# Kernel tuning notes

Hardware: AMD Instinct MI355X
Metric: run time of the kernel (lower is better)

## Reference

```python
import jax, jax.numpy as jnp
import numpy as np

N = 100000
E = 1600000
F_IN = 602
NHID = 128
N_CLS = 41


def setup_inputs() -> dict:
    key = jax.random.key(0)
    k1, k2, k3, k4 = jax.random.split(key, 4)
    x = jax.random.normal(k1, (N, F_IN), dtype=jnp.float32)
    edge_index = jax.random.randint(k2, (2, E), 0, N, dtype=jnp.int64)
    # Glorot-style scaled weights
    W1 = jax.random.normal(k3, (F_IN, NHID), dtype=jnp.float32) * (1.0 / np.sqrt(F_IN))
    b1 = jnp.zeros((NHID,), dtype=jnp.float32)
    W2 = jax.random.normal(k4, (NHID, N_CLS), dtype=jnp.float32) * (1.0 / np.sqrt(NHID))
    b2 = jnp.zeros((N_CLS,), dtype=jnp.float32)
    return {"x": x, "edge_index": edge_index, "W1": W1, "b1": b1, "W2": W2, "b2": b2}


def reference(x, edge_index, W1, b1, W2, b2):
    n = x.shape[0]
    loop = jnp.arange(n, dtype=edge_index.dtype)
    # PyG GCNConv: add self-loops, symmetric normalization D^-1/2 (A+I) D^-1/2
    src = jnp.concatenate([edge_index[0], loop])  # [E+N]
    dst = jnp.concatenate([edge_index[1], loop])  # [E+N]
    ones = jnp.ones(src.shape[0], dtype=x.dtype)
    deg = jax.ops.segment_sum(ones, dst, num_segments=n)  # in-degree incl self-loop
    dinv = jnp.where(deg > 0, jax.lax.rsqrt(deg), 0.0)
    norm = dinv[src] * dinv[dst]  # [E+N]

    def conv(h, W, b):
        h = h @ W  # transform first (smaller feature dim for gather)
        msg = h[src] * norm[:, None]  # gather + scale
        return jax.ops.segment_sum(msg, dst, num_segments=n) + b  # scatter-add

    h = jax.nn.relu(conv(x, W1, b1))
    # dropout is identity in eval mode
    out = conv(h, W2, b2)
    return jax.nn.log_softmax(out, axis=1)
```

## Files before the change

### kernel.cpp

```cpp
#include <hip/hip_runtime.h>
#include <math.h>

#define GK 602
#define GH 128
#define GC 41
#define GCP 48
#define KPAD 608
#define NKT 19

typedef __bf16 bf16x8 __attribute__((ext_vector_type(8)));
typedef float f32x16 __attribute__((ext_vector_type(16)));

__device__ __forceinline__ unsigned short f2bf(float f) {
    __bf16 b = (__bf16)f;
    return __builtin_bit_cast(unsigned short, b);
}
__device__ __forceinline__ float bf2f(unsigned short u) {
    return __uint_as_float((unsigned int)u << 16);
}
__device__ __forceinline__ float bflo(unsigned int u) { return __uint_as_float(u << 16); }
__device__ __forceinline__ float bfhi(unsigned int u) { return __uint_as_float(u & 0xffff0000u); }


__global__ void k_hist(const int* __restrict__ dst, int* __restrict__ counts, int E) {
    int e = blockIdx.x * 256 + threadIdx.x;
    if (e < E) atomicAdd(&counts[dst[e]], 1);
}

__global__ void k_scan_a(const int* __restrict__ counts, int* __restrict__ row_ptr,
                         int* __restrict__ bsum, int n) {
    __shared__ int wsum[4];
    int t = threadIdx.x;
    int lane = t & 63;
    int wv = t >> 6;
    int base = blockIdx.x * 1024 + t * 4;
    int v[4];
    int s = 0;
#pragma unroll
    for (int j = 0; j < 4; ++j) {
        int idx = base + j;
        v[j] = (idx < n) ? counts[idx] : 0;
        s += v[j];
    }
    int incl = s;
#pragma unroll
    for (int o = 1; o < 64; o <<= 1) {
        int x = __shfl_up(incl, o);
        if (lane >= o) incl += x;
    }
    if (lane == 63) wsum[wv] = incl;
    __syncthreads();
    int woff = 0;
#pragma unroll
    for (int i = 0; i < 3; ++i) woff += (i < wv) ? wsum[i] : 0;
    if (t == 255) bsum[blockIdx.x] = woff + incl;
    int off = woff + incl - s;
#pragma unroll
    for (int j = 0; j < 4; ++j) {
        int idx = base + j;
        if (idx < n) row_ptr[idx] = off;
        off += v[j];
    }
}

__global__ void k_scan_b(int* __restrict__ bsum, int nb) {
    __shared__ int sh[256];
    int t = threadIdx.x;
    int v = (t < nb) ? bsum[t] : 0;
    sh[t] = v;
    __syncthreads();
    for (int o = 1; o < 256; o <<= 1) {
        int x = (t >= o) ? sh[t - o] : 0;
        __syncthreads();
        sh[t] += x;
        __syncthreads();
    }
    if (t < nb) bsum[t] = sh[t] - v;
}

__global__ void k_scan_c(int* __restrict__ row_ptr, const int* __restrict__ bsum,
                         const int* __restrict__ counts, float* __restrict__ dinv,
                         int* __restrict__ cursor, int n, int E) {
    int i = blockIdx.x * 256 + threadIdx.x;
    if (i < n) {
        int rp = row_ptr[i] + bsum[i >> 10];
        row_ptr[i] = rp;
        cursor[i] = rp;
        dinv[i] = rsqrtf((float)(counts[i] + 1));
    }
    if (i == 0) row_ptr[n] = E;
}

__global__ void k_fill(const int* __restrict__ src, const int* __restrict__ dst,
                       const float* __restrict__ dinv,
                       int* __restrict__ cursor, int2* __restrict__ meta, int E) {
    int e = blockIdx.x * 256 + threadIdx.x;
    if (e < E) {
        int s = src[e];
        int d = dst[e];
        int p = atomicAdd(&cursor[d], 1);
        float w = dinv[s] * dinv[d];
        meta[p] = make_int2(s, __float_as_int(w));
    }
}


__global__ void k_prepW1F(const float* __restrict__ W1, unsigned short* __restrict__ W1F) {
    int i = blockIdx.x * 256 + threadIdx.x;
    if (i >= NKT * 4096) return;
    int kt = i >> 12;
    int r  = i & 4095;
    int nt = r >> 10;
    int r2 = r & 1023;
    int bs = r2 >> 9;
    int r3 = r2 & 511;
    int ln = r3 >> 3;
    int j  = r3 & 7;
    int col = 32 * nt + (ln & 31);
    int k   = 32 * kt + 16 * bs + 8 * (ln >> 5) + j;
    float v = (k < GK) ? W1[(size_t)k * GH + col] : 0.f;
    W1F[i] = f2bf(v);
}


struct AF { float4 v0, v1, v2, v3; };

__device__ __forceinline__ AF loadA(const float* __restrict__ xr, int kb, bool tail) {
    AF r;
    if (!tail) {
        r.v0 = *(const float4*)(xr + kb);
        r.v1 = *(const float4*)(xr + kb + 4);
        r.v2 = *(const float4*)(xr + kb + 16);
        r.v3 = *(const float4*)(xr + kb + 20);
    } else {
        float tv[8], tw[8];
#pragma unroll
        for (int j = 0; j < 8; ++j) {
            int k0_ = kb + j;
            int k1_ = kb + 16 + j;
            tv[j] = (k0_ < GK) ? xr[k0_] : 0.f;
            tw[j] = (k1_ < GK) ? xr[k1_] : 0.f;
        }
        r.v0 = make_float4(tv[0], tv[1], tv[2], tv[3]);
        r.v1 = make_float4(tv[4], tv[5], tv[6], tv[7]);
        r.v2 = make_float4(tw[0], tw[1], tw[2], tw[3]);
        r.v3 = make_float4(tw[4], tw[5], tw[6], tw[7]);
    }
    return r;
}

__device__ __forceinline__ bf16x8 cvt8(float4 a, float4 b) {
    bf16x8 r;
    r[0] = (__bf16)a.x; r[1] = (__bf16)a.y; r[2] = (__bf16)a.z; r[3] = (__bf16)a.w;
    r[4] = (__bf16)b.x; r[5] = (__bf16)b.y; r[6] = (__bf16)b.z; r[7] = (__bf16)b.w;
    return r;
}

__global__ __launch_bounds__(256, 4) void k_gemm1_mfma(const float* __restrict__ X,
                                                       const unsigned short* __restrict__ W1F,
                                                       unsigned short* __restrict__ Y, int M) {
    int tid = threadIdx.x;
    int lane = tid & 63;
    int w = tid >> 6;
    int rowBase = blockIdx.x * 64 + (w & 1) * 32;
    int cg = w >> 1;
    int grow_base = rowBase + (lane & 31);
    int arow = (grow_base < M) ? grow_base : (M - 1);
    const float* xr = X + (size_t)arow * GK;
    int kh = (lane >> 5) * 8;

    f32x16 acc[2];
#pragma unroll
    for (int c = 0; c < 2; ++c)
#pragma unroll
        for (int i = 0; i < 16; ++i) acc[c][i] = 0.f;

    const unsigned short* Wb = W1F + (size_t)lane * 8 + (size_t)cg * 2048;

    AF a0 = loadA(xr, kh, false);
    AF a1 = loadA(xr, kh + 32, false);

    for (int t = 0; t < NKT; ++t) {
        AF a2;
        if (t + 2 < NKT) a2 = loadA(xr, kh + 32 * (t + 2), (t + 2) == (NKT - 1));
        else             a2 = a1;

        const unsigned short* Wt = Wb + (size_t)t * 4096;
        bf16x8 af0 = cvt8(a0.v0, a0.v1);
        bf16x8 af1 = cvt8(a0.v2, a0.v3);

        bf16x8 b00 = *(const bf16x8*)(Wt);
        bf16x8 b10 = *(const bf16x8*)(Wt + 1024);
        acc[0] = __builtin_amdgcn_mfma_f32_32x32x16_bf16(af0, b00, acc[0], 0, 0, 0);
        acc[1] = __builtin_amdgcn_mfma_f32_32x32x16_bf16(af0, b10, acc[1], 0, 0, 0);

        bf16x8 b01 = *(const bf16x8*)(Wt + 512);
        bf16x8 b11 = *(const bf16x8*)(Wt + 1024 + 512);
        acc[0] = __builtin_amdgcn_mfma_f32_32x32x16_bf16(af1, b01, acc[0], 0, 0, 0);
        acc[1] = __builtin_amdgcn_mfma_f32_32x32x16_bf16(af1, b11, acc[1], 0, 0, 0);

        a0 = a1;
        a1 = a2;
    }

#pragma unroll
    for (int c = 0; c < 2; ++c) {
        int nt = 2 * cg + c;
#pragma unroll
        for (int reg = 0; reg < 16; ++reg) {
            int rrow = (reg & 3) + 8 * (reg >> 2) + 4 * (lane >> 5);
            int grow = rowBase + rrow;
            int gcol = 32 * nt + (lane & 31);
            if (grow < M) Y[(size_t)grow * GH + gcol] = f2bf(acc[c][reg]);
        }
    }
}


__global__ __launch_bounds__(256) void k_agg1(const unsigned int* __restrict__ H,
                                              unsigned int* __restrict__ O,
                                              const int* __restrict__ row_ptr,
                                              const int2* __restrict__ meta,
                                              const float* __restrict__ dinv,
                                              const float* __restrict__ bias, int n) {
    int wv = threadIdx.x >> 6;
    int lane = threadIdx.x & 63;
    int d = blockIdx.x * 4 + wv;
    if (d >= n) return;
    float dd = dinv[d];
    int beg = row_ptr[d], end = row_ptr[d + 1];
    unsigned int v = H[(size_t)d * 64 + lane];
    float sw = dd * dd;
    float a0 = sw * bflo(v);
    float a1 = sw * bfhi(v);
    int e = beg;
    for (; e + 16 <= end; e += 16) {
        int2 m[16];
        unsigned int u[16];
#pragma unroll
        for (int j = 0; j < 16; ++j) m[j] = meta[e + j];
#pragma unroll
        for (int j = 0; j < 16; ++j) u[j] = H[(size_t)m[j].x * 64 + lane];
#pragma unroll
        for (int j = 0; j < 16; ++j) {
            float wj = __int_as_float(m[j].y);
            a0 = fmaf(wj, bflo(u[j]), a0);
            a1 = fmaf(wj, bfhi(u[j]), a1);
        }
    }
    if (e + 8 <= end) {
        int2 m[8];
        unsigned int u[8];
#pragma unroll
        for (int j = 0; j < 8; ++j) m[j] = meta[e + j];
#pragma unroll
        for (int j = 0; j < 8; ++j) u[j] = H[(size_t)m[j].x * 64 + lane];
#pragma unroll
        for (int j = 0; j < 8; ++j) {
            float wj = __int_as_float(m[j].y);
            a0 = fmaf(wj, bflo(u[j]), a0);
            a1 = fmaf(wj, bfhi(u[j]), a1);
        }
        e += 8;
    }
    if (e + 4 <= end) {
        int2 m[4];
        unsigned int u[4];
#pragma unroll
        for (int j = 0; j < 4; ++j) m[j] = meta[e + j];
#pragma unroll
        for (int j = 0; j < 4; ++j) u[j] = H[(size_t)m[j].x * 64 + lane];
#pragma unroll
        for (int j = 0; j < 4; ++j) {
            float wj = __int_as_float(m[j].y);
            a0 = fmaf(wj, bflo(u[j]), a0);
            a1 = fmaf(wj, bfhi(u[j]), a1);
        }
        e += 4;
    }
    for (; e < end; ++e) {
        int2 m = meta[e];
        unsigned int u = H[(size_t)m.x * 64 + lane];
        float wj = __int_as_float(m.y);
        a0 = fmaf(wj, bflo(u), a0);
        a1 = fmaf(wj, bfhi(u), a1);
    }
    a0 = fmaxf(a0 + bias[2 * lane], 0.f);
    a1 = fmaxf(a1 + bias[2 * lane + 1], 0.f);
    O[(size_t)d * 64 + lane] = (unsigned int)f2bf(a0) | ((unsigned int)f2bf(a1) << 16);
}


__global__ __launch_bounds__(256) void k_gemm2t(const unsigned int* __restrict__ Hb,
                                                const float* __restrict__ W2,
                                                unsigned short* __restrict__ G, int n) {
    __shared__ float ws[128][GCP];
    for (int i = threadIdx.x; i < 128 * GCP; i += 256) {
        int k = i / GCP;
        int c = i - k * GCP;
        ws[k][c] = (c < GC) ? W2[k * GC + c] : 0.f;
    }
    __syncthreads();
    int r0 = blockIdx.x * 512 + threadIdx.x;
    int r1 = r0 + 256;
    bool v0 = r0 < n, v1 = r1 < n;
    float acc0[GCP], acc1[GCP];
#pragma unroll
    for (int c = 0; c < GCP; ++c) { acc0[c] = 0.f; acc1[c] = 0.f; }
    const uint2* h0 = (const uint2*)(Hb + (size_t)(v0 ? r0 : 0) * 64);
    const uint2* h1 = (const uint2*)(Hb + (size_t)(v1 ? r1 : 0) * 64);
    for (int q = 0; q < 32; ++q) {
        uint2 ua = h0[q];
        uint2 ub = h1[q];
        float va[4] = {bflo(ua.x), bfhi(ua.x), bflo(ua.y), bfhi(ua.y)};
        float vb[4] = {bflo(ub.x), bfhi(ub.x), bflo(ub.y), bfhi(ub.y)};
#pragma unroll
        for (int j = 0; j < 4; ++j) {
            int k = 4 * q + j;
#pragma unroll
            for (int cq = 0; cq < GCP / 4; ++cq) {
                float4 wv = *(const float4*)&ws[k][4 * cq];
                acc0[4 * cq + 0] = fmaf(va[j], wv.x, acc0[4 * cq + 0]);
                acc0[4 * cq + 1] = fmaf(va[j], wv.y, acc0[4 * cq + 1]);
                acc0[4 * cq + 2] = fmaf(va[j], wv.z, acc0[4 * cq + 2]);
                acc0[4 * cq + 3] = fmaf(va[j], wv.w, acc0[4 * cq + 3]);
                acc1[4 * cq + 0] = fmaf(vb[j], wv.x, acc1[4 * cq + 0]);
                acc1[4 * cq + 1] = fmaf(vb[j], wv.y, acc1[4 * cq + 1]);
                acc1[4 * cq + 2] = fmaf(vb[j], wv.z, acc1[4 * cq + 2]);
                acc1[4 * cq + 3] = fmaf(vb[j], wv.w, acc1[4 * cq + 3]);
            }
        }
    }
    if (v0) {
#pragma unroll
        for (int c = 0; c < GCP; ++c) G[(size_t)r0 * GCP + c] = f2bf(acc0[c]);
    }
    if (v1) {
#pragma unroll
        for (int c = 0; c < GCP; ++c) G[(size_t)r1 * GCP + c] = f2bf(acc1[c]);
    }
}


__global__ __launch_bounds__(256) void k_agg2(const unsigned short* __restrict__ G,
                                              float* __restrict__ out,
                                              const int* __restrict__ row_ptr,
                                              const int2* __restrict__ meta,
                                              const float* __restrict__ dinv,
                                              const float* __restrict__ b2, int n) {
    int wv = threadIdx.x >> 6;
    int lane = threadIdx.x & 63;
    int gl = (lane < GCP) ? lane : (GCP - 1);
    int d = blockIdx.x * 4 + wv;
    if (d >= n) return;
    float dd = dinv[d];
    int beg = row_ptr[d], end = row_ptr[d + 1];
    float a = dd * dd * bf2f(G[(size_t)d * GCP + gl]);
    int e = beg;
    for (; e + 16 <= end; e += 16) {
        int2 m[16];
        unsigned short u[16];
#pragma unroll
        for (int j = 0; j < 16; ++j) m[j] = meta[e + j];
#pragma unroll
        for (int j = 0; j < 16; ++j) u[j] = G[(size_t)m[j].x * GCP + gl];
#pragma unroll
        for (int j = 0; j < 16; ++j) a = fmaf(__int_as_float(m[j].y), bf2f(u[j]), a);
    }
    if (e + 8 <= end) {
        int2 m[8];
        unsigned short u[8];
#pragma unroll
        for (int j = 0; j < 8; ++j) m[j] = meta[e + j];
#pragma unroll
        for (int j = 0; j < 8; ++j) u[j] = G[(size_t)m[j].x * GCP + gl];
#pragma unroll
        for (int j = 0; j < 8; ++j) a = fmaf(__int_as_float(m[j].y), bf2f(u[j]), a);
        e += 8;
    }
    if (e + 4 <= end) {
        int2 m[4];
        unsigned short u[4];
#pragma unroll
        for (int j = 0; j < 4; ++j) m[j] = meta[e + j];
#pragma unroll
        for (int j = 0; j < 4; ++j) u[j] = G[(size_t)m[j].x * GCP + gl];
#pragma unroll
        for (int j = 0; j < 4; ++j) a = fmaf(__int_as_float(m[j].y), bf2f(u[j]), a);
        e += 4;
    }
    for (; e < end; ++e) {
        int2 m = meta[e];
        a = fmaf(__int_as_float(m.y), bf2f(G[(size_t)m.x * GCP + gl]), a);
    }
    float logit = (lane < GC) ? (a + b2[lane]) : -INFINITY;
    float mx = logit;
#pragma unroll
    for (int off = 32; off; off >>= 1) mx = fmaxf(mx, __shfl_xor(mx, off));
    float ex = (lane < GC) ? __expf(logit - mx) : 0.f;
    float sm = ex;
#pragma unroll
    for (int off = 32; off; off >>= 1) sm += __shfl_xor(sm, off);
    if (lane < GC) out[(size_t)d * GC + lane] = logit - mx - __logf(sm);
}


static inline size_t alignup256(size_t x) { return (x + 255) & ~(size_t)255; }

extern "C" void kernel_launch(void* const* d_in, const int* in_sizes, int n_in,
                              void* d_out, int out_size, void* d_ws, size_t ws_size,
                              hipStream_t stream) {
    const float* x  = (const float*)d_in[0];
    const int*   ei = (const int*)d_in[1];
    const float* W1 = (const float*)d_in[2];
    const float* b1 = (const float*)d_in[3];
    const float* W2 = (const float*)d_in[4];
    const float* b2 = (const float*)d_in[5];
    float* out = (float*)d_out;

    const int n = in_sizes[0] / GK;
    const int E = in_sizes[1] / 2;
    const int* src = ei;
    const int* dst = ei + E;

    char* w = (char*)d_ws;
    char* p;
    p = w; w += alignup256((size_t)n * 4);            float* dinv  = (float*)p;
    p = w; w += alignup256((size_t)n * 4);            int* counts  = (int*)p;
    p = w; w += alignup256((size_t)n * 4);            int* cursor  = (int*)p;
    p = w; w += alignup256((size_t)(n + 1) * 4);      int* row_ptr = (int*)p;
    p = w; w += alignup256(1024 * 4);                 int* bsum    = (int*)p;
    p = w; w += alignup256((size_t)E * 8);            int2* meta   = (int2*)p;
    p = w; w += alignup256((size_t)GH * KPAD * 2);    unsigned short* W1F = (unsigned short*)p;
    p = w; w += alignup256((size_t)n * GH * 2);       unsigned short* bufA = (unsigned short*)p;
    p = w; w += alignup256((size_t)n * GH * 2);       unsigned short* bufB = (unsigned short*)p;
    p = w; w += alignup256((size_t)n * GCP * 2);      unsigned short* G    = (unsigned short*)p;

    hipMemsetAsync(counts, 0, (size_t)n * 4, stream);

    int gE = (E + 255) / 256;
    int gN = (n + 255) / 256;
    int nb = (n + 1023) / 1024;

    k_hist<<<gE, 256, 0, stream>>>(dst, counts, E);
    k_scan_a<<<nb, 256, 0, stream>>>(counts, row_ptr, bsum, n);
    k_scan_b<<<1, 256, 0, stream>>>(bsum, nb);
    k_scan_c<<<gN, 256, 0, stream>>>(row_ptr, bsum, counts, dinv, cursor, n, E);
    k_fill<<<gE, 256, 0, stream>>>(src, dst, dinv, cursor, meta, E);

    k_prepW1F<<<(NKT * 4096 + 255) / 256, 256, 0, stream>>>(W1, W1F);
    k_gemm1_mfma<<<(n + 63) / 64, 256, 0, stream>>>(x, W1F, bufA, n);
    k_agg1<<<(n + 3) / 4, 256, 0, stream>>>((const unsigned int*)bufA, (unsigned int*)bufB,
                                            row_ptr, meta, dinv, b1, n);
    k_gemm2t<<<(n + 511) / 512, 256, 0, stream>>>((const unsigned int*)bufB, W2, G, n);
    k_agg2<<<(n + 3) / 4, 256, 0, stream>>>(G, out, row_ptr, meta, dinv, b2, n);
}
```

Before: 758.8 us.

## Stage X row slabs into LDS via direct global-to-LDS loads in GEMM1

GEMM1 now copies a contiguous 32-row slab of X (32x602 floats) into shared memory with global_load_lds, then each of 4 waves computes a distinct 32-column tile reading A from LDS. Previously each wave pair re-read X rows from global with strided per-lane loads, so every row was read twice. The new scheme reads X once with coalesced contiguous loads, at the cost of about 77KB of LDS per block, lower occupancy (2 blocks/CU), and no overlap between the load phase and the MFMA phase. The last block's slab load reads past the end of X when n is not a multiple of 32, which holds here since n=100000 is divisible by 32.

```diff
diff --git a/kernel.cpp b/kernel.cpp
--- a/kernel.cpp
+++ b/kernel.cpp
@@ -20,6 +20,15 @@
 }
 __device__ __forceinline__ float bflo(unsigned int u) { return __uint_as_float(u << 16); }
 __device__ __forceinline__ float bfhi(unsigned int u) { return __uint_as_float(u & 0xffff0000u); }
+
+__device__ __forceinline__ void gl_lds16(const float* g, float* l) {
+    __builtin_amdgcn_global_load_lds((const __attribute__((address_space(1))) void*)g,
+                                     (__attribute__((address_space(3))) void*)l, 16, 0, 0);
+}
+__device__ __forceinline__ void gl_lds4(const float* g, float* l) {
+    __builtin_amdgcn_global_load_lds((const __attribute__((address_space(1))) void*)g,
+                                     (__attribute__((address_space(3))) void*)l, 4, 0, 0);
+}
 
 
 __global__ void k_hist(const int* __restrict__ dst, int* __restrict__ counts, int E) {
@@ -123,96 +132,78 @@
 }
 
 
-struct AF { float4 v0, v1, v2, v3; };
-
-__device__ __forceinline__ AF loadA(const float* __restrict__ xr, int kb, bool tail) {
-    AF r;
-    if (!tail) {
-        r.v0 = *(const float4*)(xr + kb);
-        r.v1 = *(const float4*)(xr + kb + 4);
-        r.v2 = *(const float4*)(xr + kb + 16);
-        r.v3 = *(const float4*)(xr + kb + 20);
-    } else {
-        float tv[8], tw[8];
-#pragma unroll
-        for (int j = 0; j < 8; ++j) {
-            int k0_ = kb + j;
-            int k1_ = kb + 16 + j;
-            tv[j] = (k0_ < GK) ? xr[k0_] : 0.f;
-            tw[j] = (k1_ < GK) ? xr[k1_] : 0.f;
-        }
-        r.v0 = make_float4(tv[0], tv[1], tv[2], tv[3]);
-        r.v1 = make_float4(tv[4], tv[5], tv[6], tv[7]);
-        r.v2 = make_float4(tw[0], tw[1], tw[2], tw[3]);
-        r.v3 = make_float4(tw[4], tw[5], tw[6], tw[7]);
-    }
-    return r;
-}
-
-__device__ __forceinline__ bf16x8 cvt8(float4 a, float4 b) {
-    bf16x8 r;
-    r[0] = (__bf16)a.x; r[1] = (__bf16)a.y; r[2] = (__bf16)a.z; r[3] = (__bf16)a.w;
-    r[4] = (__bf16)b.x; r[5] = (__bf16)b.y; r[6] = (__bf16)b.z; r[7] = (__bf16)b.w;
-    return r;
-}
-
-__global__ __launch_bounds__(256, 4) void k_gemm1_mfma(const float* __restrict__ X,
+#define SLABF (32 * GK)
+#define CH16  (SLABF / 4)
+
+__global__ __launch_bounds__(256, 2) void k_gemm1_mfma(const float* __restrict__ X,
                                                        const unsigned short* __restrict__ W1F,
                                                        unsigned short* __restrict__ Y, int M) {
+    __shared__ float As[SLABF + 16];
     int tid = threadIdx.x;
     int lane = tid & 63;
     int w = tid >> 6;
-    int rowBase = blockIdx.x * 64 + (w & 1) * 32;
-    int cg = w >> 1;
-    int grow_base = rowBase + (lane & 31);
-    int arow = (grow_base < M) ? grow_base : (M - 1);
-    const float* xr = X + (size_t)arow * GK;
-    int kh = (lane >> 5) * 8;
-
-    f32x16 acc[2];
-#pragma unroll
-    for (int c = 0; c < 2; ++c)
-#pragma unroll
-        for (int i = 0; i < 16; ++i) acc[c][i] = 0.f;
-
-    const unsigned short* Wb = W1F + (size_t)lane * 8 + (size_t)cg * 2048;
-
-    AF a0 = loadA(xr, kh, false);
-    AF a1 = loadA(xr, kh + 32, false);
-
+    int rowBase = blockIdx.x * 32;
+    const float* slab = X + (size_t)rowBase * GK;
+
+#pragma unroll
+    for (int r = 0; r < 18; ++r) {
+        int c = tid + 256 * r;
+        gl_lds16(slab + 4 * c, &As[4 * c]);
+    }
+    if (w < 3) {
+        int c = 4608 + (w << 6) + lane;
+        gl_lds16(slab + 4 * c, &As[4 * c]);
+    } else {
+        int f = 19200 + lane;
+        gl_lds4(slab + f, &As[f]);
+    }
+    if (tid < 16) As[SLABF + tid] = 0.f;
+    asm volatile("s_waitcnt vmcnt(0)" ::: "memory");
+    __syncthreads();
+
+    int arow = lane & 31;
+    int kh = 8 * (lane >> 5);
+    const float* Ar = &As[arow * GK];
+    const unsigned short* Wb = W1F + (size_t)w * 1024 + (size_t)lane * 8;
+
+    f32x16 acc;
+#pragma unroll
+    for (int i = 0; i < 16; ++i) acc[i] = 0.f;
+
+#pragma unroll
     for (int t = 0; t < NKT; ++t) {
-        AF a2;
-        if (t + 2 < NKT) a2 = loadA(xr, kh + 32 * (t + 2), (t + 2) == (NKT - 1));
-        else             a2 = a1;
-
         const unsigned short* Wt = Wb + (size_t)t * 4096;
-        bf16x8 af0 = cvt8(a0.v0, a0.v1);
-        bf16x8 af1 = cvt8(a0.v2, a0.v3);
-
-        bf16x8 b00 = *(const bf16x8*)(Wt);
-        bf16x8 b10 = *(const bf16x8*)(Wt + 1024);
-        acc[0] = __builtin_amdgcn_mfma_f32_32x32x16_bf16(af0, b00, acc[0], 0, 0, 0);
-        acc[1] = __builtin_amdgcn_mfma_f32_32x32x16_bf16(af0, b10, acc[1], 0, 0, 0);
-
-        bf16x8 b01 = *(const bf16x8*)(Wt + 512);
-        bf16x8 b11 = *(const bf16x8*)(Wt + 1024 + 512);
-        acc[0] = __builtin_amdgcn_mfma_f32_32x32x16_bf16(af1, b01, acc[0], 0, 0, 0);
-        acc[1] = __builtin_amdgcn_mfma_f32_32x32x16_bf16(af1, b11, acc[1], 0, 0, 0);
-
-        a0 = a1;
-        a1 = a2;
-    }
-
-#pragma unroll
-    for (int c = 0; c < 2; ++c) {
-        int nt = 2 * cg + c;
-#pragma unroll
-        for (int reg = 0; reg < 16; ++reg) {
-            int rrow = (reg & 3) + 8 * (reg >> 2) + 4 * (lane >> 5);
-            int grow = rowBase + rrow;
-            int gcol = 32 * nt + (lane & 31);
-            if (grow < M) Y[(size_t)grow * GH + gcol] = f2bf(acc[c][reg]);
-        }
+        bf16x8 b0 = *(const bf16x8*)(Wt);
+        bf16x8 b1 = *(const bf16x8*)(Wt + 512);
+        const float* a0p = Ar + 32 * t + kh;
+        float2 p0 = *(const float2*)(a0p + 0);
+        float2 p1 = *(const float2*)(a0p + 2);
+        float2 p2 = *(const float2*)(a0p + 4);
+        float2 p3 = *(const float2*)(a0p + 6);
+        const float* a1p = a0p + 16;
+        float2 q0 = *(const float2*)(a1p + 0);
+        float2 q1 = *(const float2*)(a1p + 2);
+        float2 q2 = *(const float2*)(a1p + 4);
+        float2 q3 = *(const float2*)(a1p + 6);
+        bf16x8 af0, af1;
+        af0[0] = (__bf16)p0.x; af0[1] = (__bf16)p0.y;
+        af0[2] = (__bf16)p1.x; af0[3] = (__bf16)p1.y;
+        af0[4] = (__bf16)p2.x; af0[5] = (__bf16)p2.y;
+        af0[6] = (__bf16)p3.x; af0[7] = (__bf16)p3.y;
+        af1[0] = (__bf16)q0.x; af1[1] = (__bf16)q0.y;
+        af1[2] = (__bf16)q1.x; af1[3] = (__bf16)q1.y;
+        af1[4] = (__bf16)q2.x; af1[5] = (__bf16)q2.y;
+        af1[6] = (__bf16)q3.x; af1[7] = (__bf16)q3.y;
+        acc = __builtin_amdgcn_mfma_f32_32x32x16_bf16(af0, b0, acc, 0, 0, 0);
+        acc = __builtin_amdgcn_mfma_f32_32x32x16_bf16(af1, b1, acc, 0, 0, 0);
+    }
+
+    int gcol = 32 * w + (lane & 31);
+#pragma unroll
+    for (int reg = 0; reg < 16; ++reg) {
+        int rrow = (reg & 3) + 8 * (reg >> 2) + 4 * (lane >> 5);
+        int grow = rowBase + rrow;
+        if (grow < M) Y[(size_t)grow * GH + gcol] = f2bf(acc[reg]);
     }
 }
 
@@ -449,7 +440,7 @@
     k_fill<<<gE, 256, 0, stream>>>(src, dst, dinv, cursor, meta, E);
 
     k_prepW1F<<<(NKT * 4096 + 255) / 256, 256, 0, stream>>>(W1, W1F);
-    k_gemm1_mfma<<<(n + 63) / 64, 256, 0, stream>>>(x, W1F, bufA, n);
+    k_gemm1_mfma<<<(n + 31) / 32, 256, 0, stream>>>(x, W1F, bufA, n);
     k_agg1<<<(n + 3) / 4, 256, 0, stream>>>((const unsigned int*)bufA, (unsigned int*)bufB,
                                             row_ptr, meta, dinv, b1, n);
     k_gemm2t<<<(n + 511) / 512, 256, 0, stream>>>((const unsigned int*)bufB, W2, G, n);
```

After: 679.9 us. 10.4% less time.
